# Optimization experiments

Measured on AMD Instinct MI355X. Metric: run time of the kernel, lower is better.

Reference implementation:

```python
import jax, jax.numpy as jnp
import numpy as np

FEATURE_DIM = 128
N_NODES = 100000
N_EDGES = 800000
L1_IN = 2 * FEATURE_DIM            # 256
L1_OUT = int((2 * FEATURE_DIM) ** 0.5)  # 16
L2_DIM = L1_OUT + 1                # 17


def leaky(x):
    return jnp.where(x >= 0, x, 0.1 * x)


def setup_inputs() -> dict:
    key = jax.random.key(0)
    ks = jax.random.split(key, 8)
    Jt_ind = jax.random.randint(ks[0], (2, N_EDGES), 0, N_NODES)
    Jt_val = jax.random.normal(ks[1], (N_EDGES,), dtype=jnp.float32)
    f = jax.random.normal(ks[2], (N_NODES, FEATURE_DIM), dtype=jnp.float32)
    W1 = jax.random.normal(ks[3], (L1_IN, L1_OUT), dtype=jnp.float32) * (1.0 / np.sqrt(L1_IN))
    b1 = jnp.zeros((L1_OUT,), dtype=jnp.float32)
    W2 = jax.random.normal(ks[4], (L2_DIM, L2_DIM), dtype=jnp.float32) * (1.0 / np.sqrt(L2_DIM))
    b2 = jnp.zeros((L2_DIM,), dtype=jnp.float32)
    Wc = jax.random.normal(ks[5], (L2_DIM, 1), dtype=jnp.float32) * (1.0 / np.sqrt(L2_DIM))
    bc = jnp.ones((1,), dtype=jnp.float32)  # collapse_bias = 1
    return {"Jt_ind": Jt_ind, "Jt_val": Jt_val, "f": f, "N": N_NODES,
            "W1": W1, "b1": b1, "W2": W2, "b2": b2, "Wc": Wc, "bc": bc}


def reference(Jt_ind, Jt_val, f, N, W1, b1, W2, b2, Wc, bc):
    i = Jt_ind[0]
    j = Jt_ind[1]
    absv = jnp.abs(Jt_val)                                     # [E]
    # degree: per-destination sum of |Jt_val|
    deg_abs = jax.ops.segment_sum(absv, i, num_segments=N)     # [N]
    Jt_val_abs_norm = absv / deg_abs[i]                        # [E]
    # gather endpoint features and run tiny edge-MLP
    x = jnp.concatenate([f[i], f[j]], axis=1)                  # [E, 2F]
    x = leaky(x @ W1 + b1)                                     # [E, L1_OUT]
    x = jnp.concatenate([x, Jt_val_abs_norm[:, None]], axis=1) # [E, L2_DIM]
    x = leaky(x @ W2 + b2)                                     # [E, L2_DIM]
    e_values = (x @ Wc + bc)[:, 0]                             # [E]
    # segment softmax over edges grouped by destination i (stable)
    m = jax.ops.segment_max(e_values, i, num_segments=N)       # [N]
    ex = jnp.exp(e_values - m[i])                              # [E]
    s = jax.ops.segment_sum(ex, i, num_segments=N)             # [N]
    return ex / s[i]                                           # [E]
```

## Files before the change

kernel.cpp:

```cpp
#include <hip/hip_runtime.h>
#include <hip/hip_fp16.h>
#include <math.h>

#define FDIM  128
#define L1OUT 16
#define L2DIM 17
#define TR    64
#define TSTR  132

struct __align__(16) H16 { __half2 h[8]; };

__device__ __forceinline__ float lrelu(float v) { return v >= 0.f ? v : 0.1f * v; }

__global__ void node_transform(
    const float* __restrict__ f, const float* __restrict__ W1,
    const float* __restrict__ b1,
    const int* __restrict__ ind_i, const float* __restrict__ val,
    H16* __restrict__ A, H16* __restrict__ B,
    float* __restrict__ deg, int N, int E)
{
    __shared__ __align__(16) float tile[TR * TSTR];

    const int t    = threadIdx.x;
    const int gtid = blockIdx.x * 256 + t;
    const int GT   = gridDim.x * 256;

    {
        const int E4 = E >> 2;
        for (int q = gtid; q < E4; q += GT) {
            int e = q << 2;
            int4   ii = *reinterpret_cast<const int4*>(ind_i + e);
            float4 vv = *reinterpret_cast<const float4*>(val + e);
            atomicAdd(&deg[ii.x], fabsf(vv.x));
            atomicAdd(&deg[ii.y], fabsf(vv.y));
            atomicAdd(&deg[ii.z], fabsf(vv.z));
            atomicAdd(&deg[ii.w], fabsf(vv.w));
        }
        if (gtid < (E & 3)) {
            int e = (E & ~3) + gtid;
            atomicAdd(&deg[ind_i[e]], fabsf(val[e]));
        }
    }

    const int base = blockIdx.x * TR;
#pragma unroll
    for (int q = 0; q < 8; ++q) {
        int i4 = t + 256 * q;
        int r  = i4 >> 5;
        int c4 = i4 & 31;
        float4 v = make_float4(0.f, 0.f, 0.f, 0.f);
        if (base + r < N)
            v = reinterpret_cast<const float4*>(f + (size_t)(base + r) * FDIM)[c4];
        *reinterpret_cast<float4*>(&tile[r * TSTR + c4 * 4]) = v;
    }
    __syncthreads();

    const int lane    = t & 63;
    const int w       = t >> 6;
    const int colbase = (w & 1) * 8;
    const int isB     = w >> 1;
    const float* wbase = W1 + (size_t)(isB * FDIM) * L1OUT + colbase;

    float acc[8];
#pragma unroll
    for (int c = 0; c < 8; ++c) acc[c] = isB ? 0.f : b1[colbase + c];

    const float* trow = &tile[lane * TSTR];
#pragma unroll 2
    for (int k4 = 0; k4 < FDIM / 4; ++k4) {
        float4 xv = *reinterpret_cast<const float4*>(trow + k4 * 4);
#pragma unroll
        for (int u = 0; u < 4; ++u) {
            float x = (u == 0) ? xv.x : (u == 1) ? xv.y : (u == 2) ? xv.z : xv.w;
            const float* wr = wbase + (size_t)(k4 * 4 + u) * L1OUT;
            float4 w0  = *reinterpret_cast<const float4*>(wr);
            float4 w1v = *reinterpret_cast<const float4*>(wr + 4);
            acc[0] += x * w0.x;  acc[1] += x * w0.y;
            acc[2] += x * w0.z;  acc[3] += x * w0.w;
            acc[4] += x * w1v.x; acc[5] += x * w1v.y;
            acc[6] += x * w1v.z; acc[7] += x * w1v.w;
        }
    }

    int n = base + lane;
    if (n < N) {
        __align__(16) __half2 h[4];
#pragma unroll
        for (int q = 0; q < 4; ++q)
            h[q] = __floats2half2_rn(acc[2 * q], acc[2 * q + 1]);
        H16* arr = isB ? B : A;
        float4* dst = reinterpret_cast<float4*>(
            reinterpret_cast<char*>(arr + n) + (w & 1) * 16);
        *dst = *reinterpret_cast<float4*>(h);
    }
}

__global__ void edge_mlp(
    const int* __restrict__ ind, const float* __restrict__ val,
    const H16* __restrict__ A, const H16* __restrict__ B,
    const float* __restrict__ deg,
    const float* __restrict__ W2, const float* __restrict__ b2,
    const float* __restrict__ Wc, const float* __restrict__ bc,
    float* __restrict__ eout, float* __restrict__ ssum, int E)
{
    __shared__ float w2s[L2DIM * 20];
    __shared__ float b2s[L2DIM];
    __shared__ float wcs[L2DIM];
    __shared__ float bc0s;

    const int t = threadIdx.x;
    for (int idx = t; idx < L2DIM * L2DIM; idx += 512) {
        int c = idx / L2DIM, r = idx - c * L2DIM;
        w2s[c * 20 + r] = W2[idx];
    }
    if (t < L2DIM) b2s[t] = b2[t];
    if (t < L2DIM) wcs[t] = Wc[t];
    if (t == 0)    bc0s   = bc[0];
    __syncthreads();

    const int e = blockIdx.x * 512 + t;
    if (e >= E) return;

    int   i = ind[e];
    int   j = ind[E + e];
    H16   a  = A[i];
    H16   bb = B[j];
    float v  = val[e];
    float dg = deg[i];

    float x[L2DIM];
#pragma unroll
    for (int q = 0; q < 8; ++q) {
        float2 fa = __half22float2(a.h[q]);
        float2 fb = __half22float2(bb.h[q]);
        x[2 * q]     = lrelu(fa.x + fb.x);
        x[2 * q + 1] = lrelu(fa.y + fb.y);
    }
    x[L1OUT] = fabsf(v) / dg;

    float acc[L2DIM];
#pragma unroll
    for (int r = 0; r < L2DIM; ++r) acc[r] = b2s[r];
#pragma unroll
    for (int c = 0; c < L2DIM; ++c) {
        float xc = x[c];
        const float4* r4 = reinterpret_cast<const float4*>(&w2s[c * 20]);
        float4 w0 = r4[0], w1v = r4[1], w2v = r4[2], w3 = r4[3];
        float  w16 = w2s[c * 20 + 16];
        acc[0]  += xc * w0.x;  acc[1]  += xc * w0.y;
        acc[2]  += xc * w0.z;  acc[3]  += xc * w0.w;
        acc[4]  += xc * w1v.x; acc[5]  += xc * w1v.y;
        acc[6]  += xc * w1v.z; acc[7]  += xc * w1v.w;
        acc[8]  += xc * w2v.x; acc[9]  += xc * w2v.y;
        acc[10] += xc * w2v.z; acc[11] += xc * w2v.w;
        acc[12] += xc * w3.x;  acc[13] += xc * w3.y;
        acc[14] += xc * w3.z;  acc[15] += xc * w3.w;
        acc[16] += xc * w16;
    }
    float ev = bc0s;
#pragma unroll
    for (int r = 0; r < L2DIM; ++r) ev += lrelu(acc[r]) * wcs[r];

    float ex = __expf(ev);
    eout[e] = ex;
    atomicAdd(&ssum[i], ex);
}

__global__ void normalize(const int* __restrict__ ind_i, const float* __restrict__ ssum,
                          float* __restrict__ ex, int E) {
    int t = blockIdx.x * blockDim.x + threadIdx.x;
    int e = t * 4;
    if (e + 3 < E) {
        int4   ii = *reinterpret_cast<const int4*>(ind_i + e);
        float4 vv = *reinterpret_cast<const float4*>(ex + e);
        vv.x /= ssum[ii.x];
        vv.y /= ssum[ii.y];
        vv.z /= ssum[ii.z];
        vv.w /= ssum[ii.w];
        *reinterpret_cast<float4*>(ex + e) = vv;
    } else {
        for (; e < E; ++e) ex[e] = ex[e] / ssum[ind_i[e]];
    }
}

extern "C" void kernel_launch(void* const* d_in, const int* in_sizes, int n_in,
                              void* d_out, int out_size, void* d_ws, size_t ws_size,
                              hipStream_t stream) {
    const int*   Jt_ind = (const int*)  d_in[0];
    const float* Jt_val = (const float*)d_in[1];
    const float* f      = (const float*)d_in[2];
    const float* W1 = (const float*)d_in[4];
    const float* b1 = (const float*)d_in[5];
    const float* W2 = (const float*)d_in[6];
    const float* b2 = (const float*)d_in[7];
    const float* Wc = (const float*)d_in[8];
    const float* bc = (const float*)d_in[9];

    const int E = in_sizes[1];
    const int N = in_sizes[2] / FDIM;
    float* out = (float*)d_out;

    char* ws = (char*)d_ws;
    float* deg  = (float*)ws;  ws += (size_t)N * sizeof(float);
    float* ssum = (float*)ws;  ws += (size_t)N * sizeof(float);
    H16*   A    = (H16*)ws;    ws += (size_t)N * sizeof(H16);
    H16*   Bm   = (H16*)ws;    ws += (size_t)N * sizeof(H16);

    const int B256 = 256;
    const int B512 = 512;
    const int nblk = (N + TR - 1) / TR;
    const int eblk = (E + B512 - 1) / B512;
    const int qblk = ((E + 3) / 4 + B256 - 1) / B256;

    hipMemsetAsync(deg, 0, 2 * (size_t)N * sizeof(float), stream);
    node_transform<<<nblk, B256, 0, stream>>>(f, W1, b1, Jt_ind, Jt_val,
                                              A, Bm, deg, N, E);
    edge_mlp      <<<eblk, B512, 0, stream>>>(Jt_ind, Jt_val, A, Bm, deg,
                                              W2, b2, Wc, bc, out, ssum, E);
    normalize     <<<qblk, B256, 0, stream>>>(Jt_ind, ssum, out, E);
}
```

Before: 255.3 us.

## Compute node-level W1 projection with fp16 MFMA instead of scalar FMA

The node_transform GEMM (128x16 per half of W1) moves from per-thread scalar fp32 FMAs to 16x16x32 fp16 MFMA instructions. Each block now handles 128 nodes with the feature tile staged in LDS as fp16, and W1 fragments are held in registers. This cuts the ALU cost of the projection and halves the number of node blocks. In exchange, f and W1 are rounded to fp16 before the multiply, which adds some precision loss. The output writes become scattered 2-byte stores per lane.

```diff
diff --git a/kernel.cpp b/kernel.cpp
--- a/kernel.cpp
+++ b/kernel.cpp
@@ -5,8 +5,11 @@
 #define FDIM  128
 #define L1OUT 16
 #define L2DIM 17
-#define TR    64
-#define TSTR  132
+#define TRM   128
+#define HSTR  136
+
+typedef _Float16 f16x8 __attribute__((ext_vector_type(8)));
+typedef float    f32x4 __attribute__((ext_vector_type(4)));
 
 struct __align__(16) H16 { __half2 h[8]; };
 
@@ -19,7 +22,7 @@
     H16* __restrict__ A, H16* __restrict__ B,
     float* __restrict__ deg, int N, int E)
 {
-    __shared__ __align__(16) float tile[TR * TSTR];
+    __shared__ __align__(16) _Float16 tile[TRM * HSTR];
 
     const int t    = threadIdx.x;
     const int gtid = blockIdx.x * 256 + t;
@@ -42,56 +45,69 @@
         }
     }
 
-    const int base = blockIdx.x * TR;
+    const int lane = t & 63;
+    const int wv   = t >> 6;
+    const int n    = lane & 15;
+    const int quad = lane >> 4;
+
+    f16x8 bfr[2][4];
+#pragma unroll
+    for (int nt = 0; nt < 2; ++nt)
+#pragma unroll
+        for (int ks = 0; ks < 4; ++ks) {
+            f16x8 bf;
+#pragma unroll
+            for (int j = 0; j < 8; ++j) {
+                int k = 32 * ks + 8 * quad + j;
+                bf[j] = (_Float16)W1[(size_t)(nt * FDIM + k) * L1OUT + n];
+            }
+            bfr[nt][ks] = bf;
+        }
+    float b1v = b1[n];
+
+    const int base = blockIdx.x * TRM;
 #pragma unroll
     for (int q = 0; q < 8; ++q) {
-        int i4 = t + 256 * q;
-        int r  = i4 >> 5;
-        int c4 = i4 & 31;
-        float4 v = make_float4(0.f, 0.f, 0.f, 0.f);
-        if (base + r < N)
-            v = reinterpret_cast<const float4*>(f + (size_t)(base + r) * FDIM)[c4];
-        *reinterpret_cast<float4*>(&tile[r * TSTR + c4 * 4]) = v;
+        int p  = t + 256 * q;
+        int r  = p >> 4;
+        int c8 = p & 15;
+        float4 lo = make_float4(0.f, 0.f, 0.f, 0.f);
+        float4 hi = lo;
+        if (base + r < N) {
+            const float4* src = reinterpret_cast<const float4*>(
+                f + (size_t)(base + r) * FDIM + c8 * 8);
+            lo = src[0];
+            hi = src[1];
+        }
+        f16x8 hx;
+        hx[0] = (_Float16)lo.x; hx[1] = (_Float16)lo.y;
+        hx[2] = (_Float16)lo.z; hx[3] = (_Float16)lo.w;
+        hx[4] = (_Float16)hi.x; hx[5] = (_Float16)hi.y;
+        hx[6] = (_Float16)hi.z; hx[7] = (_Float16)hi.w;
+        *reinterpret_cast<f16x8*>(&tile[r * HSTR + c8 * 8]) = hx;
     }
     __syncthreads();
 
-    const int lane    = t & 63;
-    const int w       = t >> 6;
-    const int colbase = (w & 1) * 8;
-    const int isB     = w >> 1;
-    const float* wbase = W1 + (size_t)(isB * FDIM) * L1OUT + colbase;
-
-    float acc[8];
-#pragma unroll
-    for (int c = 0; c < 8; ++c) acc[c] = isB ? 0.f : b1[colbase + c];
-
-    const float* trow = &tile[lane * TSTR];
-#pragma unroll 2
-    for (int k4 = 0; k4 < FDIM / 4; ++k4) {
-        float4 xv = *reinterpret_cast<const float4*>(trow + k4 * 4);
-#pragma unroll
-        for (int u = 0; u < 4; ++u) {
-            float x = (u == 0) ? xv.x : (u == 1) ? xv.y : (u == 2) ? xv.z : xv.w;
-            const float* wr = wbase + (size_t)(k4 * 4 + u) * L1OUT;
-            float4 w0  = *reinterpret_cast<const float4*>(wr);
-            float4 w1v = *reinterpret_cast<const float4*>(wr + 4);
-            acc[0] += x * w0.x;  acc[1] += x * w0.y;
-            acc[2] += x * w0.z;  acc[3] += x * w0.w;
-            acc[4] += x * w1v.x; acc[5] += x * w1v.y;
-            acc[6] += x * w1v.z; acc[7] += x * w1v.w;
-        }
-    }
-
-    int n = base + lane;
-    if (n < N) {
-        __align__(16) __half2 h[4];
-#pragma unroll
-        for (int q = 0; q < 4; ++q)
-            h[q] = __floats2half2_rn(acc[2 * q], acc[2 * q + 1]);
-        H16* arr = isB ? B : A;
-        float4* dst = reinterpret_cast<float4*>(
-            reinterpret_cast<char*>(arr + n) + (w & 1) * 16);
-        *dst = *reinterpret_cast<float4*>(h);
+#pragma unroll
+    for (int si = 0; si < 2; ++si) {
+        const int m0 = (wv + 4 * si) * 16;
+        f32x4 acc0 = { b1v, b1v, b1v, b1v };
+        f32x4 acc1 = { 0.f, 0.f, 0.f, 0.f };
+#pragma unroll
+        for (int ks = 0; ks < 4; ++ks) {
+            f16x8 af = *reinterpret_cast<const f16x8*>(
+                &tile[(m0 + n) * HSTR + 32 * ks + 8 * quad]);
+            acc0 = __builtin_amdgcn_mfma_f32_16x16x32_f16(af, bfr[0][ks], acc0, 0, 0, 0);
+            acc1 = __builtin_amdgcn_mfma_f32_16x16x32_f16(af, bfr[1][ks], acc1, 0, 0, 0);
+        }
+#pragma unroll
+        for (int reg = 0; reg < 4; ++reg) {
+            int node = base + m0 + quad * 4 + reg;
+            if (node < N) {
+                reinterpret_cast<_Float16*>(A + node)[n] = (_Float16)acc0[reg];
+                reinterpret_cast<_Float16*>(B + node)[n] = (_Float16)acc1[reg];
+            }
+        }
     }
 }
 
@@ -208,7 +224,7 @@
 
     const int B256 = 256;
     const int B512 = 512;
-    const int nblk = (N + TR - 1) / TR;
+    const int nblk = (N + TRM - 1) / TRM;
     const int eblk = (E + B512 - 1) / B512;
     const int qblk = ((E + 3) / 4 + B256 - 1) / B256;
 
```

Result: faster. 211.3 us (-17.2%).
